# Optimization experiments

Hardware: AMD Instinct MI355X
Metric: run time of the kernel (lower is better)

## Reference

```python
import jax, jax.numpy as jnp
import numpy as np

# Config constants (from model_cfg)
X_RANGE = (0.0, 70.4)
Y_RANGE = (-40.0, 40.0)
Z_RANGE = (-3.0, 1.0)
RES = 0.2
Z_RES = 0.8
B, C, RH, RW = 2, 64, 64, 2048
W = int((Y_RANGE[1] - Y_RANGE[0]) / RES)   # 400
H = int((X_RANGE[1] - X_RANGE[0]) / RES)   # 352
D = int((Z_RANGE[1] - Z_RANGE[0]) / Z_RES) # 5


def setup_inputs() -> dict:
    key = jax.random.key(0)
    k1, k2, k3, k4 = jax.random.split(key, 4)
    range_res = jax.random.normal(k1, (B, C, RH, RW), dtype=jnp.float32)
    # realistic lidar xyz: x forward, y lateral, z height (slightly wider than
    # the crop ranges so clamping / z-dropping paths are exercised)
    x = jax.random.uniform(k2, (B, 1, RH, RW), minval=-5.0, maxval=75.0)
    y = jax.random.uniform(k3, (B, 1, RH, RW), minval=-45.0, maxval=45.0)
    z = jax.random.uniform(k4, (B, 1, RH, RW), minval=-3.5, maxval=1.5)
    rangemap_xyz = jnp.concatenate([x, y, z], axis=1).astype(jnp.float32)
    return {"range_res": range_res, "rangemap_xyz": rangemap_xyz, "batch_size": B}


def reference(range_res, rangemap_xyz, batch_size):
    b, c, rh, rw = range_res.shape
    n = rh * rw
    pts = rangemap_xyz.reshape(b, 3, n)            # [B,3,N]
    xp, yp, zp = pts[:, 0], pts[:, 1], pts[:, 2]   # [B,N] each
    feat = range_res.reshape(b, c, n).transpose(0, 2, 1)  # [B,N,C]

    # torch .long() truncates toward zero, as does astype(int32)
    x_img = (-yp / RES).astype(jnp.int32) - int(np.floor(Y_RANGE[0] / RES))
    y_img = (-xp / RES).astype(jnp.int32) + int(np.floor(X_RANGE[1] / RES))
    x_img = jnp.clip(x_img, 0, W - 1)
    y_img = jnp.clip(y_img, 0, H - 1)

    # height-bin index; points outside [z0, z1) are dropped (never scattered)
    zbin = jnp.floor((zp - Z_RANGE[0]) / Z_RES).astype(jnp.int32)
    valid = (zp >= Z_RANGE[0]) & (zp < Z_RANGE[1])
    zbin = jnp.where(valid, zbin, D)  # D is out-of-bounds -> mode='drop'

    # im is flipped along both spatial dims after the scatter; equivalent to
    # scattering at flipped indices.
    xf = (W - 1) - x_img
    yf = (H - 1) - y_img

    bidx = jnp.arange(b, dtype=jnp.int32)[:, None]  # [B,1] broadcast over N
    bev = jnp.zeros((b, D, W, H, c), dtype=range_res.dtype)
    bev = bev.at[bidx, zbin, xf, yf].set(feat, mode="drop")

    # original: bev [b,w,h,c,d] -> permute(0,3,4,1,2) = [b,c,d,w,h]
    # ours is [b,d,w,h,c] -> [b,c,d,w,h]
    return bev.transpose(0, 4, 1, 2, 3)
```

## Files before the change

### kernel.cpp

```cpp
#include <hip/hip_runtime.h>


namespace {

typedef float v4f __attribute__((ext_vector_type(4)));
typedef float v2f __attribute__((ext_vector_type(2)));

constexpr int Wg    = 400;
constexpr int Hg    = 352;
constexpr int Dg    = 5;
constexpr int NCELL = Dg * Wg * Hg;
constexpr int NPTS  = 64 * 2048;
constexpr int CC    = 64;
constexpr int BB    = 2;
constexpr int GRP   = 128;
constexpr int NGRP  = NCELL / GRP;
constexpr int RR    = GRP + 1;

__global__ void scatter_winner_k(const float* __restrict__ xyz,
                                 int* __restrict__ winner) {
    int idx = blockIdx.x * blockDim.x + threadIdx.x;
    if (idx >= BB * NPTS) return;
    int b = idx >> 17;
    int i = idx & (NPTS - 1);
    const float* base = xyz + (size_t)b * 3 * NPTS;
    float xp = base[i];
    float yp = base[NPTS + i];
    float zp = base[2 * NPTS + i];
    if (!(zp >= -3.0f && zp < 1.0f)) return;
    int zbin  = (int)floorf((zp + 3.0f) / 0.8f);
    int x_img = (int)(-yp / 0.2f) + 200;
    int y_img = (int)(-xp / 0.2f) + 352;
    x_img = min(max(x_img, 0), Wg - 1);
    y_img = min(max(y_img, 0), Hg - 1);
    int xf = (Wg - 1) - x_img;
    int yf = (Hg - 1) - y_img;
    int cell = (zbin * Wg + xf) * Hg + yf;
    atomicMax(winner + b * NCELL + cell, i);
}

__global__ __launch_bounds__(256) void transpose_k(const float* __restrict__ feat,
                                                   float* __restrict__ featT) {
    __shared__ float tile[64][65];
    int blk = blockIdx.x;
    int b   = blk >> 11;
    int n0  = (blk & 2047) * 64;
    const float* fb = feat  + (size_t)b * CC * NPTS;
    float*       tb = featT + (size_t)b * NPTS * CC;
    int t = threadIdx.x, w = t >> 6, l = t & 63;
    int sub = l >> 4, m = l & 15;
#pragma unroll
    for (int k = 0; k < 4; ++k) {
        int c = k * 16 + w * 4 + sub;
        v4f v = *reinterpret_cast<const v4f*>(fb + (size_t)c * NPTS + n0 + m * 4);
        tile[c][m * 4 + 0] = v.x;
        tile[c][m * 4 + 1] = v.y;
        tile[c][m * 4 + 2] = v.z;
        tile[c][m * 4 + 3] = v.w;
    }
    __syncthreads();
#pragma unroll
    for (int k = 0; k < 4; ++k) {
        int nn = k * 16 + w * 4 + sub;
        v4f v;
        v.x = tile[m * 4 + 0][nn];
        v.y = tile[m * 4 + 1][nn];
        v.z = tile[m * 4 + 2][nn];
        v.w = tile[m * 4 + 3][nn];
        *reinterpret_cast<v4f*>(tb + (size_t)(n0 + nn) * CC + m * 4) = v;
    }
}

__global__ __launch_bounds__(256) void bev_write_k(const float* __restrict__ featT,
                                                   const int*   __restrict__ winner,
                                                   float*       __restrict__ out) {
    __shared__ float tile[CC][RR];
    __shared__ int   wins[GRP];
    int blk   = blockIdx.x;
    int b     = blk / NGRP;
    int cell0 = (blk - b * NGRP) * GRP;
    int t     = threadIdx.x;
    int w     = t >> 6, l = t & 63;
    int sub   = l >> 4, m = l & 15;

    if (t < GRP) wins[t] = winner[b * NCELL + cell0 + t];
    __syncthreads();

    const float* ftb = featT + (size_t)b * NPTS * CC;
#pragma unroll
    for (int k = 0; k < 8; ++k) {
        int g  = k * 16 + w * 4 + sub;
        int pt = wins[g];
        v4f v = {0.0f, 0.0f, 0.0f, 0.0f};
        if (pt >= 0)
            v = *reinterpret_cast<const v4f*>(ftb + (size_t)pt * CC + m * 4);
        tile[m * 4 + 0][g] = v.x;
        tile[m * 4 + 1][g] = v.y;
        tile[m * 4 + 2][g] = v.z;
        tile[m * 4 + 3][g] = v.w;
    }
    __syncthreads();
    float* ob = out + (size_t)b * CC * NCELL + cell0;
#pragma unroll
    for (int k = 0; k < 16; ++k) {
        int c = k * 4 + w;
        v2f v = *reinterpret_cast<const v2f*>(&tile[c][2 * l]);
        *reinterpret_cast<v2f*>(ob + (size_t)c * NCELL + 2 * l) = v;
    }
}

}

extern "C" void kernel_launch(void* const* d_in, const int* in_sizes, int n_in,
                              void* d_out, int out_size, void* d_ws, size_t ws_size,
                              hipStream_t stream) {
    const float* range_res = (const float*)d_in[0];
    const float* xyz       = (const float*)d_in[1];
    float* out             = (float*)d_out;
    int*   winner          = (int*)d_ws;
    float* featT           = (float*)((char*)d_ws + (8u << 20));

    (void)hipMemsetAsync(winner, 0xFF, (size_t)BB * NCELL * sizeof(int), stream);

    {
        int total = BB * NPTS;
        scatter_winner_k<<<(total + 255) / 256, 256, 0, stream>>>(xyz, winner);
    }
    {
        int blocks = BB * (NPTS / 64);
        transpose_k<<<blocks, 256, 0, stream>>>(range_res, featT);
    }
    {
        int blocks = BB * NGRP;
        bev_write_k<<<blocks, 256, 0, stream>>>(featT, winner, out);
    }
}
```

Before: 468.6 us.

## Rewrite BEV write as per-channel streaming gather with nontemporal stores

The BEV output kernel no longer stages a 128-cell by 64-channel tile in shared memory. Each block now owns one (batch, channel) plane slice of about 64k cells and walks it with a grid-stride loop. For each cell it reads the winner index, gathers one float from the transposed features and writes it with a nontemporal store. This removes the shared-memory transpose and its barriers, and keeps output writes fully coalesced. The cost is that the winner array is reread once per channel (64 times), and the feature gathers become scattered scalar loads with poor sector use instead of 16-byte vectors.

```diff
diff --git a/kernel.cpp b/kernel.cpp
--- a/kernel.cpp
+++ b/kernel.cpp
@@ -4,7 +4,6 @@
 namespace {
 
 typedef float v4f __attribute__((ext_vector_type(4)));
-typedef float v2f __attribute__((ext_vector_type(2)));
 
 constexpr int Wg    = 400;
 constexpr int Hg    = 352;
@@ -13,9 +12,8 @@
 constexpr int NPTS  = 64 * 2048;
 constexpr int CC    = 64;
 constexpr int BB    = 2;
-constexpr int GRP   = 128;
-constexpr int NGRP  = NCELL / GRP;
-constexpr int RR    = GRP + 1;
+constexpr int Q     = 11;
+constexpr int CPC   = NCELL / Q;
 
 __global__ void scatter_winner_k(const float* __restrict__ xyz,
                                  int* __restrict__ winner) {
@@ -74,38 +72,24 @@
 __global__ __launch_bounds__(256) void bev_write_k(const float* __restrict__ featT,
                                                    const int*   __restrict__ winner,
                                                    float*       __restrict__ out) {
-    __shared__ float tile[CC][RR];
-    __shared__ int   wins[GRP];
-    int blk   = blockIdx.x;
-    int b     = blk / NGRP;
-    int cell0 = (blk - b * NGRP) * GRP;
-    int t     = threadIdx.x;
-    int w     = t >> 6, l = t & 63;
-    int sub   = l >> 4, m = l & 15;
+    int blk = blockIdx.x;
+    int q   = blk >> 7;
+    int bc  = blk & 127;
+    int b   = bc >> 6;
+    int c   = bc & 63;
+    int cell0 = q * CPC;
 
-    if (t < GRP) wins[t] = winner[b * NCELL + cell0 + t];
-    __syncthreads();
+    const int*   wb = winner + b * NCELL + cell0;
+    const float* ft = featT + (size_t)b * NPTS * CC + c;
+    float*       ob = out + (size_t)bc * NCELL + cell0;
 
-    const float* ftb = featT + (size_t)b * NPTS * CC;
-#pragma unroll
-    for (int k = 0; k < 8; ++k) {
-        int g  = k * 16 + w * 4 + sub;
-        int pt = wins[g];
-        v4f v = {0.0f, 0.0f, 0.0f, 0.0f};
-        if (pt >= 0)
-            v = *reinterpret_cast<const v4f*>(ftb + (size_t)pt * CC + m * 4);
-        tile[m * 4 + 0][g] = v.x;
-        tile[m * 4 + 1][g] = v.y;
-        tile[m * 4 + 2][g] = v.z;
-        tile[m * 4 + 3][g] = v.w;
-    }
-    __syncthreads();
-    float* ob = out + (size_t)b * CC * NCELL + cell0;
-#pragma unroll
-    for (int k = 0; k < 16; ++k) {
-        int c = k * 4 + w;
-        v2f v = *reinterpret_cast<const v2f*>(&tile[c][2 * l]);
-        *reinterpret_cast<v2f*>(ob + (size_t)c * NCELL + 2 * l) = v;
+#pragma unroll 4
+    for (int k = threadIdx.x; k < CPC; k += 256) {
+        int w = wb[k];
+        float v = 0.0f;
+        if (w >= 0)
+            v = ft[(size_t)w * CC];
+        __builtin_nontemporal_store(v, ob + k);
     }
 }
 
@@ -131,7 +115,7 @@
         transpose_k<<<blocks, 256, 0, stream>>>(range_res, featT);
     }
     {
-        int blocks = BB * NGRP;
+        int blocks = Q * BB * CC;
         bev_write_k<<<blocks, 256, 0, stream>>>(featT, winner, out);
     }
 }
```

After: 488.7 us. 4.3% more time.
